# Optimization experiments

Hardware: AMD Instinct MI355X
Metric: run time of the kernel (lower is better)

The kernel has to match this reference:

```python
import jax, jax.numpy as jnp
import numpy as np

B, N, K = 8, 1024, 9
T = B * N
EPS_BN = 1e-5


def _knn_idx(x, k):
    # x: [n, d] -> [n, k] indices of k nearest neighbours (self included, dist 0)
    x = jax.lax.stop_gradient(x)
    sq = jnp.sum(x * x, axis=1)
    d = sq[:, None] + sq[None, :] - 2.0 * (x @ x.T)
    return jax.lax.top_k(-d, k)[1]


def _mlp_bn(x, params):
    # PyG MLP with plain_last=True: linear->BN->ReLU for all but last layer, last is linear.
    n = len(params)
    for i, (W, b, g, be) in enumerate(params):
        x = x @ W + b
        if i < n - 1:
            mu = jnp.mean(x, axis=0)
            var = jnp.var(x, axis=0)  # biased, as torch BN (training stats)
            x = g * (x - mu) * jax.lax.rsqrt(var + EPS_BN) + be
            x = jax.nn.relu(x)
    return x


def _edge_conv(x, idx, params):
    # DynamicEdgeConv: message = MLP([x_i, x_j - x_i]), aggr='mean' over k neighbours
    n, k = idx.shape
    xj = x[idx]                                   # [n,k,c] gather
    xi = jnp.broadcast_to(x[:, None, :], xj.shape)
    e = jnp.concatenate([xi, xj - xi], axis=-1).reshape(n * k, -1)
    h = _mlp_bn(e, params)                        # [n*k, c_out]
    return h.reshape(n, k, -1).mean(axis=1)       # mean aggregation


def _dgcnn(x, c1, c3, head, lin2_W, lin2_b):
    # conv1: kNN within each graph (batch-aware)
    xb = x.reshape(B, N, -1)
    idx = jax.vmap(lambda g: _knn_idx(g, K))(xb)                 # [B,N,K] local
    idx = (idx + (jnp.arange(B) * N)[:, None, None]).reshape(T, K)
    x1 = _edge_conv(x, idx, c1)                                  # [T,128]
    # head MLP (norm=None, dropout inactive in eval)
    h = x1
    for i, (W, b) in enumerate(head):
        h = h @ W + b
        if i < len(head) - 1:
            h = jax.nn.relu(h)
    out = (h - jnp.mean(h)) / (jnp.std(h, ddof=1) + 1e-5)        # torch.std unbiased
    out = jax.nn.sigmoid(out)                                    # [T,1] gate
    xl = out * x
    xs = (1.0 - out) * x
    # conv3 called without batch -> global kNN over all T nodes
    xl = _edge_conv(xl, _knn_idx(xl, K), c3)                     # [T,16]
    xs = _edge_conv(xs, _knn_idx(xs, K), c3)
    xl = xl.reshape(B, N, -1).max(axis=1)                        # global_max_pool
    xs = xs.reshape(B, N, -1).max(axis=1)
    mass = jnp.concatenate([xl, xs], axis=1) @ lin2_W + lin2_b   # [B,1]
    return mass.flatten()


_PARAM_SHAPES = {
    'c1_W1': (8, 128), 'c1_b1': (128,), 'c1_g1': (128,), 'c1_be1': (128,),
    'c1_W2': (128, 128), 'c1_b2': (128,), 'c1_g2': (128,), 'c1_be2': (128,),
    'c1_W3': (128, 128), 'c1_b3': (128,),
    'c3_W1': (8, 64), 'c3_b1': (64,), 'c3_g1': (64,), 'c3_be1': (64,),
    'c3_W2': (64, 64), 'c3_b2': (64,), 'c3_g2': (64,), 'c3_be2': (64,),
    'c3_W3': (64, 16), 'c3_b3': (16,),
    'h_W1': (128, 64), 'h_b1': (64,),
    'h_W2': (64, 32), 'h_b2': (32,),
    'h_W3': (32, 1), 'h_b3': (1,),
    'lin2_W': (32, 1), 'lin2_b': (1,),
}


def setup_inputs() -> dict:
    key = jax.random.key(0)
    ks = jax.random.split(key, len(_PARAM_SHAPES) + 1)
    inp = {'x': jax.random.normal(ks[0], (T, 4), dtype=jnp.float32)}
    for i, (name, shp) in enumerate(_PARAM_SHAPES.items()):
        v = jax.random.normal(ks[i + 1], shp, dtype=jnp.float32) * 0.1
        if '_g' in name:
            v = v + 1.0
        inp[name] = v
    return inp


def reference(x, c1_W1, c1_b1, c1_g1, c1_be1, c1_W2, c1_b2, c1_g2, c1_be2,
              c1_W3, c1_b3, c3_W1, c3_b1, c3_g1, c3_be1, c3_W2, c3_b2, c3_g2,
              c3_be2, c3_W3, c3_b3, h_W1, h_b1, h_W2, h_b2, h_W3, h_b3,
              lin2_W, lin2_b):
    c1 = [(c1_W1, c1_b1, c1_g1, c1_be1), (c1_W2, c1_b2, c1_g2, c1_be2),
          (c1_W3, c1_b3, None, None)]
    c3 = [(c3_W1, c3_b1, c3_g1, c3_be1), (c3_W2, c3_b2, c3_g2, c3_be2),
          (c3_W3, c3_b3, None, None)]
    head = [(h_W1, h_b1), (h_W2, h_b2), (h_W3, h_b3)]
    return _dgcnn(x, c1, c3, head, lin2_W, lin2_b)
```

## Files before the change

kernel.cpp:

```cpp
#include <hip/hip_runtime.h>
#include <math.h>

#define TN 8192
#define KNN 9
#define NPG 1024
#define TK (TN*KNN)
#define CPCL 12
#define NCHG 32
#define CPCG 16
#define NSYB 768

__device__ __forceinline__ float sqnorm(float4 v){
  return fmaf(v.x,v.x,fmaf(v.y,v.y,fmaf(v.z,v.z,v.w*v.w)));
}
__device__ __forceinline__ float pairdist(float4 a, float sqa, float4 b, float sqb){
  float dot = fmaf(a.x,b.x,fmaf(a.y,b.y,fmaf(a.z,b.z,a.w*b.w)));
  return sqa + sqb - 2.0f*dot;
}
__device__ __forceinline__ void chain9(float (&bd)[9], float d){
  float t=d;
  #pragma unroll
  for(int p=0;p<9;p++){
    float lo=fminf(bd[p],t);
    t=fmaxf(bd[p],t);
    bd[p]=lo;
  }
}
__device__ __forceinline__ void insert9(float (&bd)[9], int (&bi)[9], float d, int id){
  if(d < bd[8]){
    float td=d; int ti=id;
    #pragma unroll
    for(int p=0;p<9;p++){
      bool sw = (td < bd[p]);
      float nbd = sw ? td : bd[p];
      int   nbi = sw ? ti : bi[p];
      float ntd = sw ? bd[p] : td;
      int   nti = sw ? bi[p] : ti;
      bd[p]=nbd; bi[p]=nbi; td=ntd; ti=nti;
    }
  }
}

__global__ __launch_bounds__(256) void k_part_local(const float4* __restrict__ x, float* __restrict__ pd){
  __shared__ float4 sx[128]; __shared__ float ssq[128];
  int nb = blockIdx.x >> 3, chunk = blockIdx.x & 7;
  int g = nb >> 2;
  int cbase = g*NPG + chunk*128;
  if(threadIdx.x < 128){
    float4 v = x[cbase + threadIdx.x];
    sx[threadIdx.x]=v; ssq[threadIdx.x]=sqnorm(v);
  }
  __syncthreads();
  int node = nb*256 + threadIdx.x;
  float4 xi = x[node]; float sqi = sqnorm(xi);
  float bdA[9], bdB[9];
  #pragma unroll
  for(int q=0;q<9;q++){bdA[q]=1e30f;bdB[q]=1e30f;}
  for(int j=0;j<128;j+=2){
    chain9(bdA, pairdist(xi,sqi,sx[j],ssq[j]));
    chain9(bdB, pairdist(xi,sqi,sx[j+1],ssq[j+1]));
  }
  #pragma unroll
  for(int q=0;q<9;q++) chain9(bdA, bdB[q]);
  #pragma unroll
  for(int q=0;q<9;q++) pd[(size_t)(chunk*9+q)*TN + node]=bdA[q];
}

__global__ __launch_bounds__(256) void k_thresh_local(const float* __restrict__ pd,
      float* __restrict__ tl){
  int node = blockIdx.x*256 + threadIdx.x;
  float bd[9];
  #pragma unroll
  for(int q=0;q<9;q++) bd[q]=1e30f;
  for(int m=0;m<72;m++) chain9(bd, pd[(size_t)m*TN + node]);
  float t = bd[8];
  tl[node] = t + fabsf(t)*1e-5f + 1e-12f;
}

__global__ __launch_bounds__(256) void k_collect_local(const float4* __restrict__ x,
      const float* __restrict__ tl, unsigned char* __restrict__ cnt8,
      unsigned short* __restrict__ list){
  __shared__ float4 sx[128]; __shared__ float ssq[128];
  int nb = blockIdx.x >> 3, chunk = blockIdx.x & 7;
  int g = nb >> 2;
  int cbase = g*NPG + chunk*128;
  if(threadIdx.x < 128){
    float4 v = x[cbase + threadIdx.x];
    sx[threadIdx.x]=v; ssq[threadIdx.x]=sqnorm(v);
  }
  __syncthreads();
  int node = nb*256 + threadIdx.x;
  float4 xi = x[node];
  float m2x=-2.0f*xi.x, m2y=-2.0f*xi.y, m2z=-2.0f*xi.z, m2w=-2.0f*xi.w;
  float tadj = tl[node] - sqnorm(xi);
  int cnt = 0;
  unsigned short* lst = list + ((size_t)node*8 + chunk)*CPCL;
  for(int j=0;j<128;j+=4){
    float4 v0=sx[j], v1=sx[j+1], v2=sx[j+2], v3=sx[j+3];
    float q0=ssq[j], q1=ssq[j+1], q2=ssq[j+2], q3=ssq[j+3];
    float s0=fmaf(v0.x,m2x,fmaf(v0.y,m2y,fmaf(v0.z,m2z,fmaf(v0.w,m2w,q0))));
    float s1=fmaf(v1.x,m2x,fmaf(v1.y,m2y,fmaf(v1.z,m2z,fmaf(v1.w,m2w,q1))));
    float s2=fmaf(v2.x,m2x,fmaf(v2.y,m2y,fmaf(v2.z,m2z,fmaf(v2.w,m2w,q2))));
    float s3=fmaf(v3.x,m2x,fmaf(v3.y,m2y,fmaf(v3.z,m2z,fmaf(v3.w,m2w,q3))));
    if(s0<=tadj){ if(cnt<CPCL) lst[cnt]=(unsigned short)(cbase+j  ); cnt++; }
    if(s1<=tadj){ if(cnt<CPCL) lst[cnt]=(unsigned short)(cbase+j+1); cnt++; }
    if(s2<=tadj){ if(cnt<CPCL) lst[cnt]=(unsigned short)(cbase+j+2); cnt++; }
    if(s3<=tadj){ if(cnt<CPCL) lst[cnt]=(unsigned short)(cbase+j+3); cnt++; }
  }
  cnt8[(size_t)node*8 + chunk] = (unsigned char)(cnt > 255 ? 255 : cnt);
}

__global__ __launch_bounds__(256) void k_refine_local(const float4* __restrict__ x,
      const unsigned char* __restrict__ cnt8, const unsigned short* __restrict__ list,
      int* __restrict__ out){
  __shared__ float sval[32][73];
  __shared__ int   sidx[32][73];
  __shared__ int   sovf[32];
  int slot = threadIdx.x >> 3, sub = threadIdx.x & 7;
  int node = blockIdx.x*32 + slot;
  if(sub==0) sovf[slot]=0;
  __syncthreads();
  float4 xi = x[node]; float sqi = sqnorm(xi);
  float bd[9]; int bi[9];
  #pragma unroll
  for(int q=0;q<9;q++){bd[q]=1e30f; bi[q]=node;}
  int ch = sub;
  int c = cnt8[(size_t)node*8 + ch];
  if(c > CPCL) sovf[slot]=1;
  int n = c < CPCL ? c : CPCL;
  const unsigned short* lst = list + ((size_t)node*8 + ch)*CPCL;
  for(int m=0;m<n;m++){
    int j = lst[m]; float4 v = x[j];
    insert9(bd,bi, pairdist(xi,sqi,v,sqnorm(v)), j);
  }
  #pragma unroll
  for(int q=0;q<9;q++){ sval[slot][sub*9+q]=bd[q]; sidx[slot][sub*9+q]=bi[q]; }
  __syncthreads();
  if(sub==0){
    for(int m=9;m<72;m++) insert9(bd,bi, sval[slot][m], sidx[slot][m]);
    if(sovf[slot]){
      #pragma unroll
      for(int q=0;q<9;q++){bd[q]=1e30f; bi[q]=node;}
      int gbase = node & ~(NPG-1);
      for(int j=gbase;j<gbase+NPG;j++){
        float4 v = x[j];
        insert9(bd,bi, pairdist(xi,sqi,v,sqnorm(v)), j);
      }
    }
    #pragma unroll
    for(int q=0;q<9;q++) out[(size_t)node*9+q]=bi[q];
  }
}

__global__ __launch_bounds__(256) void k_part_sub(const float4* __restrict__ xa,
      const float4* __restrict__ xb, float* __restrict__ pd){
  const float4* x = blockIdx.y ? xb : xa;
  __shared__ float4 sx[256]; __shared__ float ssq[256];
  int nb = blockIdx.x >> 3, chunk = blockIdx.x & 7;
  {
    int j = (chunk*256 + threadIdx.x)*4;
    float4 v = x[j];
    sx[threadIdx.x]=v; ssq[threadIdx.x]=sqnorm(v);
  }
  __syncthreads();
  int node = nb*256 + threadIdx.x;
  float4 xi = x[node]; float sqi = sqnorm(xi);
  float bdA[9], bdB[9];
  #pragma unroll
  for(int q=0;q<9;q++){bdA[q]=1e30f;bdB[q]=1e30f;}
  for(int j=0;j<256;j+=2){
    chain9(bdA, pairdist(xi,sqi,sx[j],ssq[j]));
    chain9(bdB, pairdist(xi,sqi,sx[j+1],ssq[j+1]));
  }
  #pragma unroll
  for(int q=0;q<9;q++) chain9(bdA, bdB[q]);
  int pn = blockIdx.y*TN + node;
  #pragma unroll
  for(int q=0;q<9;q++) pd[(size_t)(chunk*9+q)*2*TN + pn]=bdA[q];
}

__global__ __launch_bounds__(256) void k_thresh_sub(const float* __restrict__ pd,
      float* __restrict__ tg){
  int pn = blockIdx.x*256 + threadIdx.x;
  float bd[9];
  #pragma unroll
  for(int q=0;q<9;q++) bd[q]=1e30f;
  for(int m=0;m<72;m++) chain9(bd, pd[(size_t)m*2*TN + pn]);
  float t = bd[8];
  tg[pn] = t + fabsf(t)*1e-5f + 1e-12f;
}

__global__ __launch_bounds__(256) void k_collect_glob(const float4* __restrict__ xa,
      const float4* __restrict__ xb, const float* __restrict__ tg,
      unsigned char* __restrict__ cnt8, unsigned short* __restrict__ list){
  const float4* x = blockIdx.y ? xb : xa;
  __shared__ float4 sx[256];
  __shared__ float4 ssq4[64];
  int nb = blockIdx.x >> 5, chunk = blockIdx.x & 31;
  int cbase = chunk*256;
  {
    float4 v = x[cbase+threadIdx.x];
    sx[threadIdx.x]=v; ((float*)ssq4)[threadIdx.x]=sqnorm(v);
  }
  __syncthreads();
  int node0 = nb*512 + threadIdx.x;
  int node1 = node0 + 256;
  int pn0 = blockIdx.y*TN + node0;
  int pn1 = pn0 + 256;
  float4 xi0 = x[node0], xi1 = x[node1];
  float a0x=-2.0f*xi0.x, a0y=-2.0f*xi0.y, a0z=-2.0f*xi0.z, a0w=-2.0f*xi0.w;
  float a1x=-2.0f*xi1.x, a1y=-2.0f*xi1.y, a1z=-2.0f*xi1.z, a1w=-2.0f*xi1.w;
  float t0 = tg[pn0] - sqnorm(xi0);
  float t1 = tg[pn1] - sqnorm(xi1);
  int c0 = 0, c1 = 0;
  unsigned short* l0 = list + ((size_t)pn0*NCHG + chunk)*CPCG;
  unsigned short* l1 = list + ((size_t)pn1*NCHG + chunk)*CPCG;
  for(int j=0;j<256;j+=4){
    float4 v0=sx[j], v1=sx[j+1], v2=sx[j+2], v3=sx[j+3];
    float4 qv = ssq4[j>>2];
    float s00=fmaf(v0.x,a0x,fmaf(v0.y,a0y,fmaf(v0.z,a0z,fmaf(v0.w,a0w,qv.x))));
    float s01=fmaf(v1.x,a0x,fmaf(v1.y,a0y,fmaf(v1.z,a0z,fmaf(v1.w,a0w,qv.y))));
    float s02=fmaf(v2.x,a0x,fmaf(v2.y,a0y,fmaf(v2.z,a0z,fmaf(v2.w,a0w,qv.z))));
    float s03=fmaf(v3.x,a0x,fmaf(v3.y,a0y,fmaf(v3.z,a0z,fmaf(v3.w,a0w,qv.w))));
    float s10=fmaf(v0.x,a1x,fmaf(v0.y,a1y,fmaf(v0.z,a1z,fmaf(v0.w,a1w,qv.x))));
    float s11=fmaf(v1.x,a1x,fmaf(v1.y,a1y,fmaf(v1.z,a1z,fmaf(v1.w,a1w,qv.y))));
    float s12=fmaf(v2.x,a1x,fmaf(v2.y,a1y,fmaf(v2.z,a1z,fmaf(v2.w,a1w,qv.z))));
    float s13=fmaf(v3.x,a1x,fmaf(v3.y,a1y,fmaf(v3.z,a1z,fmaf(v3.w,a1w,qv.w))));
    if(s00<=t0){ if(c0<CPCG) l0[c0]=(unsigned short)(cbase+j  ); c0++; }
    if(s01<=t0){ if(c0<CPCG) l0[c0]=(unsigned short)(cbase+j+1); c0++; }
    if(s02<=t0){ if(c0<CPCG) l0[c0]=(unsigned short)(cbase+j+2); c0++; }
    if(s03<=t0){ if(c0<CPCG) l0[c0]=(unsigned short)(cbase+j+3); c0++; }
    if(s10<=t1){ if(c1<CPCG) l1[c1]=(unsigned short)(cbase+j  ); c1++; }
    if(s11<=t1){ if(c1<CPCG) l1[c1]=(unsigned short)(cbase+j+1); c1++; }
    if(s12<=t1){ if(c1<CPCG) l1[c1]=(unsigned short)(cbase+j+2); c1++; }
    if(s13<=t1){ if(c1<CPCG) l1[c1]=(unsigned short)(cbase+j+3); c1++; }
  }
  cnt8[(size_t)pn0*NCHG + chunk] = (unsigned char)(c0 > 255 ? 255 : c0);
  cnt8[(size_t)pn1*NCHG + chunk] = (unsigned char)(c1 > 255 ? 255 : c1);
}

__global__ __launch_bounds__(256) void k_refine_glob(const float4* __restrict__ xa,
      const float4* __restrict__ xb, const unsigned char* __restrict__ cnt8,
      const unsigned short* __restrict__ list, int* __restrict__ outl, int* __restrict__ outs){
  __shared__ float sval[32][73];
  __shared__ int   sidx[32][73];
  __shared__ int   sovf[32];
  int slot = threadIdx.x >> 3, sub = threadIdx.x & 7;
  int pn = blockIdx.x*32 + slot;
  int prob = blockIdx.x >> 8;
  int node = pn & (TN-1);
  const float4* x = prob ? xb : xa;
  if(sub==0) sovf[slot]=0;
  __syncthreads();
  float4 xi = x[node]; float sqi = sqnorm(xi);
  float bd[9]; int bi[9];
  #pragma unroll
  for(int q=0;q<9;q++){bd[q]=1e30f; bi[q]=node;}
  bool ovf=false;
  for(int ch=sub*4; ch<sub*4+4; ch++){
    int c = cnt8[(size_t)pn*NCHG + ch];
    if(c > CPCG) ovf=true;
    int n = c < CPCG ? c : CPCG;
    const unsigned short* lst = list + ((size_t)pn*NCHG + ch)*CPCG;
    for(int m=0;m<n;m++){
      int j = lst[m]; float4 v = x[j];
      insert9(bd,bi, pairdist(xi,sqi,v,sqnorm(v)), j);
    }
  }
  if(ovf) sovf[slot]=1;
  #pragma unroll
  for(int q=0;q<9;q++){ sval[slot][sub*9+q]=bd[q]; sidx[slot][sub*9+q]=bi[q]; }
  __syncthreads();
  if(sub==0){
    for(int m=9;m<72;m++) insert9(bd,bi, sval[slot][m], sidx[slot][m]);
    if(sovf[slot]){
      #pragma unroll
      for(int q=0;q<9;q++){bd[q]=1e30f; bi[q]=node;}
      for(int j=0;j<TN;j++){
        float4 v = x[j];
        insert9(bd,bi, pairdist(xi,sqi,v,sqnorm(v)), j);
      }
    }
    int* o = prob ? outs : outl;
    #pragma unroll
    for(int q=0;q<9;q++) o[(size_t)node*9+q]=bi[q];
  }
}

__global__ __launch_bounds__(256) void k_mom8(const float4* __restrict__ x,
      const int* __restrict__ idx, float* __restrict__ mpart){
  __shared__ float sa[256][9];
  int t = threadIdx.x;
  int e = blockIdx.x*256 + t;
  int i = e/KNN; int j = idx[e];
  float4 xi = x[i], xj = x[j];
  sa[t][0]=xi.x; sa[t][1]=xi.y; sa[t][2]=xi.z; sa[t][3]=xi.w;
  sa[t][4]=xj.x-xi.x; sa[t][5]=xj.y-xi.y; sa[t][6]=xj.z-xi.z; sa[t][7]=xj.w-xi.w;
  __syncthreads();
  if(t < 44){
    float s=0.f;
    if(t<8){
      for(int e2=0;e2<256;e2++) s += sa[e2][t];
    } else {
      int f=t-8, p=0, q=0, acc=0;
      for(p=0;p<8;p++){ int cnt=8-p; if(f<acc+cnt){ q=p+(f-acc); break;} acc+=cnt; }
      for(int e2=0;e2<256;e2++) s += sa[e2][p]*sa[e2][q];
    }
    mpart[blockIdx.x*44+t]=s;
  }
}

__global__ void k_bn1q(const float* __restrict__ mpart, const float* __restrict__ W1,
      const float* __restrict__ g, const float* __restrict__ be,
      float* __restrict__ scale, float* __restrict__ shift){
  __shared__ double mom[44];
  int t = threadIdx.x;
  if(t<44){ double s=0; for(int b=0;b<288;b++) s+=(double)mpart[b*44+t]; mom[t]=s; }
  __syncthreads();
  double m[8], w[8];
  #pragma unroll
  for(int p=0;p<8;p++){ m[p]=mom[p]/(double)TK; w[p]=(double)W1[p*128+t]; }
  double q=0.0; int f=8;
  for(int p=0;p<8;p++)
    for(int qq=p;qq<8;qq++){
      double cov = mom[f]/(double)TK - m[p]*m[qq];
      q += (p==qq?1.0:2.0)*w[p]*w[qq]*cov;
      f++;
    }
  if(q<0) q=0;
  double sc = (double)g[t]/sqrt(q+1e-5);
  double mu=0; for(int p=0;p<8;p++) mu += m[p]*w[p];
  scale[t]=(float)sc;
  shift[t]=(float)((double)be[t] - mu*sc);
}

__global__ __launch_bounds__(256) void k_syrk128(const float4* __restrict__ x,
      const int* __restrict__ idx, const float* __restrict__ W1,
      const float* __restrict__ sc1, const float* __restrict__ sh1,
      float* __restrict__ mpartM){
  __shared__ float sa[48][9];
  __shared__ float sW1[8*128];
  __shared__ float sZ[48*132];
  __shared__ float ssum[128];
  const int tid = threadIdx.x;
  ((float4*)sW1)[tid] = ((const float4*)W1)[tid];
  if(tid<128) ssum[tid]=0.f;
  const int zc4 = tid & 31, ze0 = tid >> 5;
  const int gi = tid >> 4, gj = tid & 15;
  const int ia = gi*4, ib = 64 + gi*4;
  const int ja = gj*4, jb = 64 + gj*4;
  float acc[8][8];
  #pragma unroll
  for(int a=0;a<8;a++)
    #pragma unroll
    for(int b=0;b<8;b++) acc[a][b]=0.f;
  float ls[4]={0,0,0,0};
  float4 scv = ((const float4*)sc1)[zc4];
  float4 shv = ((const float4*)sh1)[zc4];
  for(int pass=0;pass<2;pass++){
    __syncthreads();
    if(tid<48){
      int e = blockIdx.x*96 + pass*48 + tid;
      int i = e/KNN; int j = idx[e];
      float4 xi = x[i], xj = x[j];
      sa[tid][0]=xi.x; sa[tid][1]=xi.y; sa[tid][2]=xi.z; sa[tid][3]=xi.w;
      sa[tid][4]=xj.x-xi.x; sa[tid][5]=xj.y-xi.y; sa[tid][6]=xj.z-xi.z; sa[tid][7]=xj.w-xi.w;
    }
    __syncthreads();
    for(int e=ze0; e<48; e+=8){
      float4 y = make_float4(0.f,0.f,0.f,0.f);
      #pragma unroll
      for(int k=0;k<8;k++){
        float a = sa[e][k];
        float4 wv = *(const float4*)(sW1 + k*128 + zc4*4);
        y.x=fmaf(a,wv.x,y.x); y.y=fmaf(a,wv.y,y.y);
        y.z=fmaf(a,wv.z,y.z); y.w=fmaf(a,wv.w,y.w);
      }
      float4 z;
      z.x = fmaxf(fmaf(scv.x,y.x,shv.x),0.f);
      z.y = fmaxf(fmaf(scv.y,y.y,shv.y),0.f);
      z.z = fmaxf(fmaf(scv.z,y.z,shv.z),0.f);
      z.w = fmaxf(fmaf(scv.w,y.w,shv.w),0.f);
      *(float4*)(sZ + e*132 + zc4*4) = z;
      ls[0]+=z.x; ls[1]+=z.y; ls[2]+=z.z; ls[3]+=z.w;
    }
    __syncthreads();
    #pragma unroll 2
    for(int e=0;e<48;e++){
      const float* rz = sZ + e*132;
      float4 zi0 = *(const float4*)(rz + ia);
      float4 zi1 = *(const float4*)(rz + ib);
      float4 zj0 = *(const float4*)(rz + ja);
      float4 zj1 = *(const float4*)(rz + jb);
      float zi[8] = {zi0.x,zi0.y,zi0.z,zi0.w,zi1.x,zi1.y,zi1.z,zi1.w};
      float zj[8] = {zj0.x,zj0.y,zj0.z,zj0.w,zj1.x,zj1.y,zj1.z,zj1.w};
      #pragma unroll
      for(int a=0;a<8;a++)
        #pragma unroll
        for(int b=0;b<8;b++) acc[a][b]=fmaf(zi[a],zj[b],acc[a][b]);
    }
  }
  #pragma unroll
  for(int c=0;c<4;c++) atomicAdd(&ssum[zc4*4+c], ls[c]);
  float* mp = mpartM + (size_t)blockIdx.x*16512;
  #pragma unroll
  for(int a=0;a<8;a++){
    int row = (a<4) ? (ia+a) : (ib+a-4);
    *(float4*)(mp + row*128 + ja) = make_float4(acc[a][0],acc[a][1],acc[a][2],acc[a][3]);
    *(float4*)(mp + row*128 + jb) = make_float4(acc[a][4],acc[a][5],acc[a][6],acc[a][7]);
  }
  __syncthreads();
  if(tid<128) mp[16384+tid] = ssum[tid];
}

__global__ __launch_bounds__(256) void k_redA(const float* __restrict__ mpartM,
      double* __restrict__ pp8){
  int ch = blockIdx.x*256 + threadIdx.x;
  if(ch >= 16512) return;
  int y = blockIdx.y;
  double s=0;
  for(int b=y*96;b<y*96+96;b++) s += (double)mpartM[(size_t)b*16512 + ch];
  pp8[(size_t)y*16512 + ch]=s;
}

__global__ __launch_bounds__(256) void k_redB(const double* __restrict__ pp8,
      double* __restrict__ Md){
  int ch = blockIdx.x*256 + threadIdx.x;
  if(ch >= 16512) return;
  double s=0;
  #pragma unroll
  for(int y=0;y<8;y++) s += pp8[(size_t)y*16512 + ch];
  Md[ch]=s;
}

__global__ void k_bn2q(const double* __restrict__ Md, const float* __restrict__ W2,
      const float* __restrict__ g, const float* __restrict__ be,
      float* __restrict__ scale, float* __restrict__ shift){
  __shared__ double redq[128], redt[128];
  __shared__ float sw[128];
  int c = blockIdx.x, t = threadIdx.x;
  sw[t] = W2[t*128+c];
  __syncthreads();
  double zb = Md[16384+t]/(double)TK;
  double inner=0;
  for(int j=0;j<128;j++) inner += Md[t*128+j]*(double)sw[j];
  redq[t] = (double)sw[t]*(inner/(double)TK);
  redt[t] = (double)sw[t]*zb;
  __syncthreads();
  for(int s=64;s>0;s>>=1){
    if(t<s){ redq[t]+=redq[t+s]; redt[t]+=redt[t+s]; }
    __syncthreads();
  }
  if(t==0){
    double var = redq[0] - redt[0]*redt[0];
    if(var<0) var=0;
    double sc = (double)g[c]/sqrt(var+1e-5);
    scale[c]=(float)sc;
    shift[c]=(float)((double)be[c] - redt[0]*sc);
  }
}

__global__ __launch_bounds__(256) void k_midagg(const float4* __restrict__ x,
      const int* __restrict__ idx, const float* __restrict__ W1,
      const float* __restrict__ sc1, const float* __restrict__ sh1,
      const float* __restrict__ W2, const float* __restrict__ sc2,
      const float* __restrict__ sh2, const float* __restrict__ W3,
      const float* __restrict__ b3, float* __restrict__ x1){
  __shared__ float sa[72][9];
  __shared__ float sW1[8*128];
  __shared__ float sZ[72*68];
  const int tid = threadIdx.x;
  const int node0 = blockIdx.x*8;
  ((float4*)sW1)[tid] = ((const float4*)W1)[tid];
  if(tid<72){
    int e = blockIdx.x*72 + tid;
    int i = e/KNN; int j = idx[e];
    float4 xi = x[i], xj = x[j];
    sa[tid][0]=xi.x; sa[tid][1]=xi.y; sa[tid][2]=xi.z; sa[tid][3]=xi.w;
    sa[tid][4]=xj.x-xi.x; sa[tid][5]=xj.y-xi.y; sa[tid][6]=xj.z-xi.z; sa[tid][7]=xj.w-xi.w;
  }
  __syncthreads();
  const int tc = tid & 31, tr = tid >> 5;
  float acc[9][4];
  #pragma unroll
  for(int s=0;s<9;s++)
    #pragma unroll
    for(int e=0;e<4;e++) acc[s][e]=0.f;
  for(int half=0; half<2; half++){
    for(int f=tid; f<72*16; f+=256){
      int e = f>>4, c4 = f&15;
      int gc4 = half*16 + c4;
      float4 scv = ((const float4*)sc1)[gc4];
      float4 shv = ((const float4*)sh1)[gc4];
      float4 y = make_float4(0.f,0.f,0.f,0.f);
      #pragma unroll
      for(int k=0;k<8;k++){
        float a = sa[e][k];
        float4 wv = *(const float4*)(sW1 + k*128 + gc4*4);
        y.x=fmaf(a,wv.x,y.x); y.y=fmaf(a,wv.y,y.y);
        y.z=fmaf(a,wv.z,y.z); y.w=fmaf(a,wv.w,y.w);
      }
      float4 z;
      z.x = fmaxf(fmaf(scv.x,y.x,shv.x),0.f);
      z.y = fmaxf(fmaf(scv.y,y.y,shv.y),0.f);
      z.z = fmaxf(fmaf(scv.z,y.z,shv.z),0.f);
      z.w = fmaxf(fmaf(scv.w,y.w,shv.w),0.f);
      *(float4*)(sZ + e*68 + c4*4) = z;
    }
    __syncthreads();
    #pragma unroll 2
    for(int k4=0;k4<16;k4++){
      float4 av[9];
      #pragma unroll
      for(int s=0;s<9;s++) av[s] = *(const float4*)(sZ + (tr*9+s)*68 + k4*4);
      #pragma unroll
      for(int kk=0;kk<4;kk++){
        float4 bv = *(const float4*)(W2 + (size_t)(half*64 + k4*4+kk)*128 + tc*4);
        #pragma unroll
        for(int s=0;s<9;s++){
          float a = (kk==0)?av[s].x:(kk==1)?av[s].y:(kk==2)?av[s].z:av[s].w;
          acc[s][0]=fmaf(a,bv.x,acc[s][0]);
          acc[s][1]=fmaf(a,bv.y,acc[s][1]);
          acc[s][2]=fmaf(a,bv.z,acc[s][2]);
          acc[s][3]=fmaf(a,bv.w,acc[s][3]);
        }
      }
    }
    __syncthreads();
  }
  float4 scv = ((const float4*)sc2)[tc];
  float4 shv = ((const float4*)sh2)[tc];
  float4 sum = make_float4(0.f,0.f,0.f,0.f);
  #pragma unroll
  for(int s=0;s<9;s++){
    sum.x += fmaxf(fmaf(scv.x,acc[s][0],shv.x),0.f);
    sum.y += fmaxf(fmaf(scv.y,acc[s][1],shv.y),0.f);
    sum.z += fmaxf(fmaf(scv.z,acc[s][2],shv.z),0.f);
    sum.w += fmaxf(fmaf(scv.w,acc[s][3],shv.w),0.f);
  }
  sum.x*=(1.f/9.f); sum.y*=(1.f/9.f); sum.z*=(1.f/9.f); sum.w*=(1.f/9.f);
  *(float4*)(sZ + tr*132 + tc*4) = sum;
  __syncthreads();
  const float* zr = sZ + tr*132;
  float4 o = make_float4(0.f,0.f,0.f,0.f);
  #pragma unroll 4
  for(int k=0;k<128;k++){
    float a = zr[k];
    float4 bv = *(const float4*)(W3 + (size_t)k*128 + tc*4);
    o.x=fmaf(a,bv.x,o.x); o.y=fmaf(a,bv.y,o.y);
    o.z=fmaf(a,bv.z,o.z); o.w=fmaf(a,bv.w,o.w);
  }
  float4 bb = ((const float4*)b3)[tc];
  o.x+=bb.x; o.y+=bb.y; o.z+=bb.z; o.w+=bb.w;
  *(float4*)(x1 + (size_t)(node0+tr)*128 + tc*4) = o;
}

__global__ __launch_bounds__(256) void k_mom8d(const float4* __restrict__ xa,
      const float4* __restrict__ xb, const int* __restrict__ ia,
      const int* __restrict__ ib, float* __restrict__ mpart){
  __shared__ float sa[256][9];
  const int prob = blockIdx.y;
  const float4* x = prob ? xb : xa;
  const int* idx = prob ? ib : ia;
  int t = threadIdx.x;
  int e = blockIdx.x*256 + t;
  int i = e/KNN; int j = idx[e];
  float4 xi = x[i], xj = x[j];
  sa[t][0]=xi.x; sa[t][1]=xi.y; sa[t][2]=xi.z; sa[t][3]=xi.w;
  sa[t][4]=xj.x-xi.x; sa[t][5]=xj.y-xi.y; sa[t][6]=xj.z-xi.z; sa[t][7]=xj.w-xi.w;
  __syncthreads();
  if(t < 44){
    float s=0.f;
    if(t<8){
      for(int e2=0;e2<256;e2++) s += sa[e2][t];
    } else {
      int f=t-8, p=0, q=0, acc=0;
      for(p=0;p<8;p++){ int cnt=8-p; if(f<acc+cnt){ q=p+(f-acc); break;} acc+=cnt; }
      for(int e2=0;e2<256;e2++) s += sa[e2][p]*sa[e2][q];
    }
    mpart[((size_t)prob*288 + blockIdx.x)*44 + t]=s;
  }
}

__global__ void k_bn1qd(const float* __restrict__ mpart, const float* __restrict__ W1,
      const float* __restrict__ g, const float* __restrict__ be,
      float* __restrict__ scale, float* __restrict__ shift){
  __shared__ double mom[2][44];
  int t = threadIdx.x;
  if(t<88){
    int pr=t/44, m=t%44;
    double s=0; for(int b=0;b<288;b++) s+=(double)mpart[((size_t)pr*288+b)*44+m];
    mom[pr][m]=s;
  }
  __syncthreads();
  int prob = t>>6, c = t&63;
  double m[8], w[8];
  #pragma unroll
  for(int p=0;p<8;p++){ m[p]=mom[prob][p]/(double)TK; w[p]=(double)W1[p*64+c]; }
  double q=0.0; int f=8;
  for(int p=0;p<8;p++)
    for(int qq=p;qq<8;qq++){
      double cov = mom[prob][f]/(double)TK - m[p]*m[qq];
      q += (p==qq?1.0:2.0)*w[p]*w[qq]*cov;
      f++;
    }
  if(q<0) q=0;
  double sc = (double)g[c]/sqrt(q+1e-5);
  double mu=0; for(int p=0;p<8;p++) mu += m[p]*w[p];
  scale[prob*64+c]=(float)sc;
  shift[prob*64+c]=(float)((double)be[c] - mu*sc);
}

__global__ __launch_bounds__(256) void k_syrk64d(const float4* __restrict__ xa,
      const float4* __restrict__ xb, const int* __restrict__ ia,
      const int* __restrict__ ib, const float* __restrict__ W1,
      const float* __restrict__ sc0, const float* __restrict__ sh0,
      float* __restrict__ mpartM){
  __shared__ float sa[64][9];
  __shared__ float sW1[8*64];
  __shared__ float sZ[64*68];
  __shared__ float ssum[64];
  const int prob = blockIdx.y;
  const float4* x = prob ? xb : xa;
  const int* idx = prob ? ib : ia;
  const float* sc1 = sc0 + prob*64;
  const float* sh1 = sh0 + prob*64;
  const int tid = threadIdx.x;
  if(tid<128) ((float4*)sW1)[tid] = ((const float4*)W1)[tid];
  if(tid<64) ssum[tid]=0.f;
  const int zc4 = tid & 15, ze0 = tid >> 4;
  const int i0 = (tid>>4)*4, j0 = (tid&15)*4;
  float acc[4][4];
  #pragma unroll
  for(int a=0;a<4;a++)
    #pragma unroll
    for(int b=0;b<4;b++) acc[a][b]=0.f;
  float ls[4]={0,0,0,0};
  float4 scv = ((const float4*)sc1)[zc4];
  float4 shv = ((const float4*)sh1)[zc4];
  for(int pass=0;pass<4;pass++){
    __syncthreads();
    if(tid<64){
      int e = blockIdx.x*256 + pass*64 + tid;
      int i = e/KNN; int j = idx[e];
      float4 xi = x[i], xj = x[j];
      sa[tid][0]=xi.x; sa[tid][1]=xi.y; sa[tid][2]=xi.z; sa[tid][3]=xi.w;
      sa[tid][4]=xj.x-xi.x; sa[tid][5]=xj.y-xi.y; sa[tid][6]=xj.z-xi.z; sa[tid][7]=xj.w-xi.w;
    }
    __syncthreads();
    for(int e=ze0; e<64; e+=16){
      float4 y = make_float4(0.f,0.f,0.f,0.f);
      #pragma unroll
      for(int k=0;k<8;k++){
        float a = sa[e][k];
        float4 wv = *(const float4*)(sW1 + k*64 + zc4*4);
        y.x=fmaf(a,wv.x,y.x); y.y=fmaf(a,wv.y,y.y);
        y.z=fmaf(a,wv.z,y.z); y.w=fmaf(a,wv.w,y.w);
      }
      float4 z;
      z.x = fmaxf(fmaf(scv.x,y.x,shv.x),0.f);
      z.y = fmaxf(fmaf(scv.y,y.y,shv.y),0.f);
      z.z = fmaxf(fmaf(scv.z,y.z,shv.z),0.f);
      z.w = fmaxf(fmaf(scv.w,y.w,shv.w),0.f);
      *(float4*)(sZ + e*68 + zc4*4) = z;
      ls[0]+=z.x; ls[1]+=z.y; ls[2]+=z.z; ls[3]+=z.w;
    }
    __syncthreads();
    #pragma unroll 4
    for(int e=0;e<64;e++){
      const float* rz = sZ + e*68;
      float4 zi4 = *(const float4*)(rz + i0);
      float4 zj4 = *(const float4*)(rz + j0);
      float zi[4]={zi4.x,zi4.y,zi4.z,zi4.w};
      float zj[4]={zj4.x,zj4.y,zj4.z,zj4.w};
      #pragma unroll
      for(int a=0;a<4;a++)
        #pragma unroll
        for(int b=0;b<4;b++) acc[a][b]=fmaf(zi[a],zj[b],acc[a][b]);
    }
  }
  #pragma unroll
  for(int c=0;c<4;c++) atomicAdd(&ssum[zc4*4+c], ls[c]);
  float* mp = mpartM + ((size_t)prob*288 + blockIdx.x)*4160;
  #pragma unroll
  for(int a=0;a<4;a++)
    *(float4*)(mp + (i0+a)*64 + j0) = make_float4(acc[a][0],acc[a][1],acc[a][2],acc[a][3]);
  __syncthreads();
  if(tid<64) mp[4096+tid] = ssum[tid];
}

__global__ __launch_bounds__(256) void k_redMd(const float* __restrict__ mpartM,
      double* __restrict__ Md){
  int ch = blockIdx.x*256 + threadIdx.x;
  if(ch >= 8320) return;
  int prob = ch / 4160, c = ch % 4160;
  double s=0;
  for(int b=0;b<288;b++) s += (double)mpartM[((size_t)prob*288+b)*4160 + c];
  Md[(size_t)prob*4160 + c]=s;
}

__global__ void k_bn2qd(const double* __restrict__ Md, const float* __restrict__ W2,
      const float* __restrict__ g, const float* __restrict__ be,
      float* __restrict__ scale, float* __restrict__ shift){
  __shared__ double redq[64], redt[64];
  __shared__ float sw[64];
  int c = blockIdx.x, prob = blockIdx.y, t = threadIdx.x;
  const double* md = Md + (size_t)prob*4160;
  sw[t] = W2[t*64+c];
  __syncthreads();
  double zb = md[4096+t]/(double)TK;
  double inner=0;
  for(int j=0;j<64;j++) inner += md[t*64+j]*(double)sw[j];
  redq[t] = (double)sw[t]*(inner/(double)TK);
  redt[t] = (double)sw[t]*zb;
  __syncthreads();
  for(int s=32;s>0;s>>=1){
    if(t<s){ redq[t]+=redq[t+s]; redt[t]+=redt[t+s]; }
    __syncthreads();
  }
  if(t==0){
    double var = redq[0] - redt[0]*redt[0];
    if(var<0) var=0;
    double sc = (double)g[c]/sqrt(var+1e-5);
    scale[prob*64+c]=(float)sc;
    shift[prob*64+c]=(float)((double)be[c] - redt[0]*sc);
  }
}

__global__ __launch_bounds__(256) void k_midagg64d(const float4* __restrict__ xa,
      const float4* __restrict__ xb, const int* __restrict__ ia,
      const int* __restrict__ ib, const float* __restrict__ W1,
      const float* __restrict__ sc0, const float* __restrict__ sh0,
      const float* __restrict__ W2, const float* __restrict__ sc20,
      const float* __restrict__ sh20, const float* __restrict__ W3,
      const float* __restrict__ b3, float* __restrict__ outl, float* __restrict__ outs){
  __shared__ float sa[144][9];
  __shared__ float sW1[8*64];
  __shared__ float sZ[144*36];
  const int prob = blockIdx.y;
  const float4* x = prob ? xb : xa;
  const int* idx = prob ? ib : ia;
  const float* sc1 = sc0 + prob*64;
  const float* sh1 = sh0 + prob*64;
  const float* sc2 = sc20 + prob*64;
  const float* sh2 = sh20 + prob*64;
  float* out = prob ? outs : outl;
  const int tid = threadIdx.x;
  const int node0 = blockIdx.x*16;
  if(tid<128) ((float4*)sW1)[tid] = ((const float4*)W1)[tid];
  if(tid<144){
    int e = blockIdx.x*144 + tid;
    int i = e/KNN; int j = idx[e];
    float4 xi = x[i], xj = x[j];
    sa[tid][0]=xi.x; sa[tid][1]=xi.y; sa[tid][2]=xi.z; sa[tid][3]=xi.w;
    sa[tid][4]=xj.x-xi.x; sa[tid][5]=xj.y-xi.y; sa[tid][6]=xj.z-xi.z; sa[tid][7]=xj.w-xi.w;
  }
  __syncthreads();
  const int cg = tid & 15, nd = tid >> 4;
  float acc[9][4];
  #pragma unroll
  for(int s=0;s<9;s++)
    #pragma unroll
    for(int e=0;e<4;e++) acc[s][e]=0.f;
  for(int half=0; half<2; half++){
    for(int f=tid; f<144*8; f+=256){
      int e = f>>3, c4 = f&7;
      int gc4 = half*8 + c4;
      float4 scv = ((const float4*)sc1)[gc4];
      float4 shv = ((const float4*)sh1)[gc4];
      float4 y = make_float4(0.f,0.f,0.f,0.f);
      #pragma unroll
      for(int k=0;k<8;k++){
        float a = sa[e][k];
        float4 wv = *(const float4*)(sW1 + k*64 + gc4*4);
        y.x=fmaf(a,wv.x,y.x); y.y=fmaf(a,wv.y,y.y);
        y.z=fmaf(a,wv.z,y.z); y.w=fmaf(a,wv.w,y.w);
      }
      float4 z;
      z.x = fmaxf(fmaf(scv.x,y.x,shv.x),0.f);
      z.y = fmaxf(fmaf(scv.y,y.y,shv.y),0.f);
      z.z = fmaxf(fmaf(scv.z,y.z,shv.z),0.f);
      z.w = fmaxf(fmaf(scv.w,y.w,shv.w),0.f);
      *(float4*)(sZ + e*36 + c4*4) = z;
    }
    __syncthreads();
    #pragma unroll 2
    for(int k4=0;k4<8;k4++){
      float4 av[9];
      #pragma unroll
      for(int s=0;s<9;s++) av[s] = *(const float4*)(sZ + (nd*9+s)*36 + k4*4);
      #pragma unroll
      for(int kk=0;kk<4;kk++){
        float4 bv = *(const float4*)(W2 + (size_t)(half*32 + k4*4+kk)*64 + cg*4);
        #pragma unroll
        for(int s=0;s<9;s++){
          float a = (kk==0)?av[s].x:(kk==1)?av[s].y:(kk==2)?av[s].z:av[s].w;
          acc[s][0]=fmaf(a,bv.x,acc[s][0]);
          acc[s][1]=fmaf(a,bv.y,acc[s][1]);
          acc[s][2]=fmaf(a,bv.z,acc[s][2]);
          acc[s][3]=fmaf(a,bv.w,acc[s][3]);
        }
      }
    }
    __syncthreads();
  }
  float4 scv = ((const float4*)sc2)[cg];
  float4 shv = ((const float4*)sh2)[cg];
  float4 sum = make_float4(0.f,0.f,0.f,0.f);
  #pragma unroll
  for(int s=0;s<9;s++){
    sum.x += fmaxf(fmaf(scv.x,acc[s][0],shv.x),0.f);
    sum.y += fmaxf(fmaf(scv.y,acc[s][1],shv.y),0.f);
    sum.z += fmaxf(fmaf(scv.z,acc[s][2],shv.z),0.f);
    sum.w += fmaxf(fmaf(scv.w,acc[s][3],shv.w),0.f);
  }
  sum.x*=(1.f/9.f); sum.y*=(1.f/9.f); sum.z*=(1.f/9.f); sum.w*=(1.f/9.f);
  *(float4*)(sZ + nd*68 + cg*4) = sum;
  __syncthreads();
  {
    int node = tid >> 4, col = tid & 15;
    const float* zr = sZ + node*68;
    float o = 0.f;
    #pragma unroll 4
    for(int k=0;k<64;k++) o = fmaf(zr[k], W3[k*16+col], o);
    out[(size_t)(node0+node)*16 + col] = o + b3[col];
  }
}

__global__ __launch_bounds__(256) void k_head(const float* __restrict__ x1,
    const float* __restrict__ W1, const float* __restrict__ b1,
    const float* __restrict__ W2, const float* __restrict__ b2,
    const float* __restrict__ W3, const float* __restrict__ b3,
    float* __restrict__ h, float* __restrict__ pstat){
  __shared__ float sA[32*132];
  __shared__ float sW1[128*64];
  __shared__ float o1[32*68];
  __shared__ float sW2[64*32];
  __shared__ float o2[32*33];
  __shared__ float sb1[64], sb2[32], sW3v[32];
  __shared__ float rs[32], rq[32];
  const int tid = threadIdx.x;
  const int row0 = blockIdx.x*32;
  for(int e=tid; e<32*32; e+=256){
    int r = e>>5, c4 = e&31;
    ((float4*)(sA + r*132))[c4] = ((const float4*)(x1 + (size_t)(row0+r)*128))[c4];
  }
  for(int e=tid; e<128*64/4; e+=256) ((float4*)sW1)[e] = ((const float4*)W1)[e];
  for(int e=tid; e<64*32/4; e+=256)  ((float4*)sW2)[e] = ((const float4*)W2)[e];
  if(tid < 64) sb1[tid]=b1[tid];
  if(tid < 32){ sb2[tid]=b2[tid]; sW3v[tid]=W3[tid]; }
  __syncthreads();
  const int tc = tid & 15, tr = tid >> 4;
  float a1[2][4];
  #pragma unroll
  for(int rr=0;rr<2;rr++)
    #pragma unroll
    for(int e=0;e<4;e++) a1[rr][e]=0.f;
  for(int k4=0;k4<32;k4++){
    float4 av0 = *(const float4*)(sA + (tr*2  )*132 + k4*4);
    float4 av1 = *(const float4*)(sA + (tr*2+1)*132 + k4*4);
    #pragma unroll
    for(int kk=0;kk<4;kk++){
      float4 bv = *(const float4*)(sW1 + (k4*4+kk)*64 + tc*4);
      float p0 = (kk==0)?av0.x:(kk==1)?av0.y:(kk==2)?av0.z:av0.w;
      float p1 = (kk==0)?av1.x:(kk==1)?av1.y:(kk==2)?av1.z:av1.w;
      a1[0][0]=fmaf(p0,bv.x,a1[0][0]); a1[0][1]=fmaf(p0,bv.y,a1[0][1]);
      a1[0][2]=fmaf(p0,bv.z,a1[0][2]); a1[0][3]=fmaf(p0,bv.w,a1[0][3]);
      a1[1][0]=fmaf(p1,bv.x,a1[1][0]); a1[1][1]=fmaf(p1,bv.y,a1[1][1]);
      a1[1][2]=fmaf(p1,bv.z,a1[1][2]); a1[1][3]=fmaf(p1,bv.w,a1[1][3]);
    }
  }
  #pragma unroll
  for(int rr=0;rr<2;rr++)
    #pragma unroll
    for(int e=0;e<4;e++)
      o1[(tr*2+rr)*68 + tc*4+e] = fmaxf(a1[rr][e]+sb1[tc*4+e], 0.f);
  __syncthreads();
  float a2[2][2] = {{0.f,0.f},{0.f,0.f}};
  for(int k=0;k<64;k++){
    float w0 = sW2[k*32 + tc*2], w1 = sW2[k*32 + tc*2+1];
    float v0 = o1[(tr*2  )*68 + k];
    float v1 = o1[(tr*2+1)*68 + k];
    a2[0][0]=fmaf(v0,w0,a2[0][0]); a2[0][1]=fmaf(v0,w1,a2[0][1]);
    a2[1][0]=fmaf(v1,w0,a2[1][0]); a2[1][1]=fmaf(v1,w1,a2[1][1]);
  }
  #pragma unroll
  for(int rr=0;rr<2;rr++)
    #pragma unroll
    for(int cc=0;cc<2;cc++)
      o2[(tr*2+rr)*33 + tc*2+cc] = fmaxf(a2[rr][cc]+sb2[tc*2+cc], 0.f);
  __syncthreads();
  if(tid < 32){
    float hv = b3[0];
    #pragma unroll
    for(int k=0;k<32;k++) hv = fmaf(o2[tid*33+k], sW3v[k], hv);
    h[row0+tid]=hv;
    rs[tid]=hv; rq[tid]=hv*hv;
  }
  __syncthreads();
  if(tid==0){
    float S=0.f, Q=0.f;
    #pragma unroll
    for(int i=0;i<32;i++){ S+=rs[i]; Q+=rq[i]; }
    pstat[blockIdx.x*2]=S; pstat[blockIdx.x*2+1]=Q;
  }
}

__global__ __launch_bounds__(256) void k_fin_h(const float* __restrict__ pstat,
      float* __restrict__ hpar){
  __shared__ double sS[256], sQ[256];
  int t = threadIdx.x;
  sS[t] = (double)pstat[2*t]; sQ[t] = (double)pstat[2*t+1];
  __syncthreads();
  for(int s=128;s>0;s>>=1){
    if(t<s){ sS[t]+=sS[t+s]; sQ[t]+=sQ[t+s]; }
    __syncthreads();
  }
  if(t==0){
    double mu = sS[0]/8192.0;
    double var = (sQ[0] - 8192.0*mu*mu)/8191.0;
    double sd = (var > 0) ? sqrt(var) : 0.0;
    hpar[0]=(float)mu;
    hpar[1]=(float)(1.0/(sd + 1e-5));
  }
}

__global__ __launch_bounds__(256) void k_gate(const float* __restrict__ h,
      const float* __restrict__ hpar, const float4* __restrict__ x,
      float4* __restrict__ xl, float4* __restrict__ xs){
  int i = blockIdx.x*256 + threadIdx.x;
  float z = (h[i]-hpar[0])*hpar[1];
  float o = 1.0f/(1.0f+expf(-z));
  float om = 1.0f - o;
  float4 v = x[i];
  xl[i] = make_float4(o*v.x, o*v.y, o*v.z, o*v.w);
  xs[i] = make_float4(om*v.x, om*v.y, om*v.z, om*v.w);
}

__global__ __launch_bounds__(256) void k_final(const float* __restrict__ xlf,
      const float* __restrict__ xsf, const float* __restrict__ W,
      const float* __restrict__ b, float* __restrict__ out){
  __shared__ float red[32][8];
  int g = blockIdx.x;
  int c = threadIdx.x & 31;
  int chunk = threadIdx.x >> 5;
  const float* src = (c < 16) ? xlf : xsf;
  int ch = (c < 16) ? c : c-16;
  float m = -1e30f;
  for(int n=chunk*128; n<chunk*128+128; n++)
    m = fmaxf(m, src[((size_t)g*1024+n)*16 + ch]);
  red[c][chunk]=m;
  __syncthreads();
  if(threadIdx.x < 32){
    float mm = red[threadIdx.x][0];
    #pragma unroll
    for(int p=1;p<8;p++) mm = fmaxf(mm, red[threadIdx.x][p]);
    red[threadIdx.x][0]=mm;
  }
  __syncthreads();
  if(threadIdx.x == 0){
    float acc = b[0];
    for(int cc=0;cc<32;cc++) acc = fmaf(red[cc][0], W[cc], acc);
    out[g]=acc;
  }
}

extern "C" void kernel_launch(void* const* d_in, const int* in_sizes, int n_in,
                              void* d_out, int out_size, void* d_ws, size_t ws_size,
                              hipStream_t stream){
  const float* x    =(const float*)d_in[0];
  const float* c1W1 =(const float*)d_in[1];
  const float* c1g1 =(const float*)d_in[3];
  const float* c1be1=(const float*)d_in[4];
  const float* c1W2 =(const float*)d_in[5];
  const float* c1g2 =(const float*)d_in[7];
  const float* c1be2=(const float*)d_in[8];
  const float* c1W3 =(const float*)d_in[9];
  const float* c1b3 =(const float*)d_in[10];
  const float* c3W1 =(const float*)d_in[11];
  const float* c3g1 =(const float*)d_in[13];
  const float* c3be1=(const float*)d_in[14];
  const float* c3W2 =(const float*)d_in[15];
  const float* c3g2 =(const float*)d_in[17];
  const float* c3be2=(const float*)d_in[18];
  const float* c3W3 =(const float*)d_in[19];
  const float* c3b3 =(const float*)d_in[20];
  const float* hW1  =(const float*)d_in[21];
  const float* hb1  =(const float*)d_in[22];
  const float* hW2  =(const float*)d_in[23];
  const float* hb2  =(const float*)d_in[24];
  const float* hW3  =(const float*)d_in[25];
  const float* hb3  =(const float*)d_in[26];
  const float* l2W  =(const float*)d_in[27];
  const float* l2b  =(const float*)d_in[28];
  (void)in_sizes; (void)n_in; (void)out_size; (void)ws_size;

  char* wsb=(char*)d_ws;
  size_t off=0;
  auto alloc=[&](size_t bytes)->char*{
    char* p = wsb + off;
    off = (off + bytes + 255) & ~(size_t)255;
    return p;
  };
  float* ovl  =(float*)alloc((size_t)NSYB*16512*4);
  float* x1   =(float*)alloc((size_t)TN*128*4);
  int*   idx1 =(int*)  alloc((size_t)TK*4);
  int*   idxl =(int*)  alloc((size_t)TK*4);
  int*   idxs =(int*)  alloc((size_t)TK*4);
  float* pd   =(float*)alloc((size_t)2*TN*72*4);
  float* h    =(float*)alloc((size_t)TN*4);
  float* xl   =(float*)alloc((size_t)TN*16);
  float* xs   =(float*)alloc((size_t)TN*16);
  float* xlf  =(float*)alloc((size_t)TN*16*4);
  float* xsf  =(float*)alloc((size_t)TN*16*4);
  float* pstat=(float*)alloc((size_t)512*4);
  double* Md  =(double*)alloc((size_t)16512*8);
  double* Mdd =(double*)alloc((size_t)8320*8);
  double* pp8 =(double*)alloc((size_t)8*16512*8);
  float* mp44 =(float*)alloc((size_t)288*44*4);
  float* mp44d=(float*)alloc((size_t)2*288*44*4);
  float* tl   =(float*)alloc((size_t)TN*4);
  float* tg   =(float*)alloc((size_t)2*TN*4);
  unsigned char* cnt8l=(unsigned char*)alloc((size_t)TN*8);
  unsigned char* cnt8g=(unsigned char*)alloc((size_t)2*TN*NCHG);
  float* bnp  =(float*)alloc(1024*4);
  float* hpar =(float*)alloc(64);

  float* sc1=bnp,      *sh1=bnp+128, *sc2=bnp+256, *sh2=bnp+384;
  float* scA=bnp+512,  *shA=bnp+640, *scB=bnp+768, *shB=bnp+896;
  unsigned short* listl=(unsigned short*)ovl;
  unsigned short* listg=(unsigned short*)ovl;
  float* mpartM = ovl;
  float* mpartMd = ovl;

  k_part_local  <<<256,256,0,stream>>>((const float4*)x, pd);
  k_thresh_local<<<32, 256,0,stream>>>(pd, tl);
  k_collect_local<<<256,256,0,stream>>>((const float4*)x, tl, cnt8l, listl);
  k_refine_local<<<TN/32,256,0,stream>>>((const float4*)x, cnt8l, listl, idx1);
  k_mom8<<<288,256,0,stream>>>((const float4*)x, idx1, mp44);
  k_bn1q<<<1,128,0,stream>>>(mp44, c1W1, c1g1, c1be1, sc1, sh1);
  k_syrk128<<<NSYB,256,0,stream>>>((const float4*)x, idx1, c1W1, sc1, sh1, mpartM);
  k_redA<<<dim3(65,8),256,0,stream>>>(mpartM, pp8);
  k_redB<<<65,256,0,stream>>>(pp8, Md);
  k_bn2q<<<128,128,0,stream>>>(Md, c1W2, c1g2, c1be2, sc2, sh2);
  k_midagg<<<1024,256,0,stream>>>((const float4*)x, idx1, c1W1, sc1, sh1, c1W2, sc2, sh2, c1W3, c1b3, x1);
  k_head<<<TN/32,256,0,stream>>>(x1,hW1,hb1,hW2,hb2,hW3,hb3,h,pstat);
  k_fin_h<<<1,256,0,stream>>>(pstat,hpar);
  k_gate<<<32,256,0,stream>>>(h,hpar,(const float4*)x,(float4*)xl,(float4*)xs);
  k_part_sub   <<<dim3(256,2),256,0,stream>>>((const float4*)xl,(const float4*)xs,pd);
  k_thresh_sub <<<64,256,0,stream>>>(pd,tg);
  k_collect_glob<<<dim3(512,2),256,0,stream>>>((const float4*)xl,(const float4*)xs,tg,cnt8g,listg);
  k_refine_glob<<<2*TN/32,256,0,stream>>>((const float4*)xl,(const float4*)xs,cnt8g,listg,idxl,idxs);
  k_mom8d<<<dim3(288,2),256,0,stream>>>((const float4*)xl,(const float4*)xs,idxl,idxs,mp44d);
  k_bn1qd<<<1,128,0,stream>>>(mp44d, c3W1, c3g1, c3be1, scA, shA);
  k_syrk64d<<<dim3(288,2),256,0,stream>>>((const float4*)xl,(const float4*)xs,idxl,idxs,c3W1,scA,shA,mpartMd);
  k_redMd<<<33,256,0,stream>>>(mpartMd, Mdd);
  k_bn2qd<<<dim3(64,2),64,0,stream>>>(Mdd, c3W2, c3g2, c3be2, scB, shB);
  k_midagg64d<<<dim3(512,2),256,0,stream>>>((const float4*)xl,(const float4*)xs,idxl,idxs,
      c3W1, scA, shA, c3W2, scB, shB, c3W3, c3b3, xlf, xsf);
  k_final<<<8,256,0,stream>>>(xlf,xsf,l2W,l2b,(float*)d_out);
}
```

Before: 407.8 us.

## Retile k_midagg to 16 nodes per block with 8 output columns per thread

k_midagg now handles 16 nodes (144 edges) per block instead of 8, and each thread computes 8 output channels for one node instead of 4. The hidden layer is processed in four 32-channel quarters rather than two 64-channel halves, which shrinks the shared staging buffer. The aim is to halve the W2/W3 global reads per edge and raise FMA work per load. In exchange each thread holds twice the accumulators (72 floats), which raises register pressure, and the grid shrinks to 512 blocks.

Result: no change. 409.8 us (+0.5%).

```diff
diff --git a/kernel.cpp b/kernel.cpp
--- a/kernel.cpp
+++ b/kernel.cpp
@@ -466,30 +466,30 @@
       const float* __restrict__ W2, const float* __restrict__ sc2,
       const float* __restrict__ sh2, const float* __restrict__ W3,
       const float* __restrict__ b3, float* __restrict__ x1){
-  __shared__ float sa[72][9];
+  __shared__ float sa[144][9];
   __shared__ float sW1[8*128];
-  __shared__ float sZ[72*68];
+  __shared__ float sZ[144*36];
   const int tid = threadIdx.x;
-  const int node0 = blockIdx.x*8;
+  const int node0 = blockIdx.x*16;
   ((float4*)sW1)[tid] = ((const float4*)W1)[tid];
-  if(tid<72){
-    int e = blockIdx.x*72 + tid;
+  if(tid<144){
+    int e = blockIdx.x*144 + tid;
     int i = e/KNN; int j = idx[e];
     float4 xi = x[i], xj = x[j];
     sa[tid][0]=xi.x; sa[tid][1]=xi.y; sa[tid][2]=xi.z; sa[tid][3]=xi.w;
     sa[tid][4]=xj.x-xi.x; sa[tid][5]=xj.y-xi.y; sa[tid][6]=xj.z-xi.z; sa[tid][7]=xj.w-xi.w;
   }
   __syncthreads();
-  const int tc = tid & 31, tr = tid >> 5;
-  float acc[9][4];
+  const int cg = tid & 15, nd = tid >> 4;
+  float acc[9][8];
   #pragma unroll
   for(int s=0;s<9;s++)
     #pragma unroll
-    for(int e=0;e<4;e++) acc[s][e]=0.f;
-  for(int half=0; half<2; half++){
-    for(int f=tid; f<72*16; f+=256){
-      int e = f>>4, c4 = f&15;
-      int gc4 = half*16 + c4;
+    for(int e=0;e<8;e++) acc[s][e]=0.f;
+  for(int q=0;q<4;q++){
+    for(int f=tid; f<144*8; f+=256){
+      int e = f>>3, c4 = f&7;
+      int gc4 = q*8 + c4;
       float4 scv = ((const float4*)sc1)[gc4];
       float4 shv = ((const float4*)sh1)[gc4];
       float4 y = make_float4(0.f,0.f,0.f,0.f);
@@ -505,54 +505,76 @@
       z.y = fmaxf(fmaf(scv.y,y.y,shv.y),0.f);
       z.z = fmaxf(fmaf(scv.z,y.z,shv.z),0.f);
       z.w = fmaxf(fmaf(scv.w,y.w,shv.w),0.f);
-      *(float4*)(sZ + e*68 + c4*4) = z;
+      *(float4*)(sZ + e*36 + c4*4) = z;
     }
     __syncthreads();
     #pragma unroll 2
-    for(int k4=0;k4<16;k4++){
-      float4 av[9];
-      #pragma unroll
-      for(int s=0;s<9;s++) av[s] = *(const float4*)(sZ + (tr*9+s)*68 + k4*4);
+    for(int k4=0;k4<8;k4++){
+      float4 bv0[4], bv1[4];
       #pragma unroll
       for(int kk=0;kk<4;kk++){
-        float4 bv = *(const float4*)(W2 + (size_t)(half*64 + k4*4+kk)*128 + tc*4);
+        const float* wr = W2 + (size_t)(q*32 + k4*4 + kk)*128 + cg*8;
+        bv0[kk] = *(const float4*)(wr);
+        bv1[kk] = *(const float4*)(wr + 4);
+      }
+      #pragma unroll
+      for(int s=0;s<9;s++){
+        float4 av = *(const float4*)(sZ + (nd*9+s)*36 + k4*4);
         #pragma unroll
-        for(int s=0;s<9;s++){
-          float a = (kk==0)?av[s].x:(kk==1)?av[s].y:(kk==2)?av[s].z:av[s].w;
-          acc[s][0]=fmaf(a,bv.x,acc[s][0]);
-          acc[s][1]=fmaf(a,bv.y,acc[s][1]);
-          acc[s][2]=fmaf(a,bv.z,acc[s][2]);
-          acc[s][3]=fmaf(a,bv.w,acc[s][3]);
+        for(int kk=0;kk<4;kk++){
+          float a = (kk==0)?av.x:(kk==1)?av.y:(kk==2)?av.z:av.w;
+          acc[s][0]=fmaf(a,bv0[kk].x,acc[s][0]);
+          acc[s][1]=fmaf(a,bv0[kk].y,acc[s][1]);
+          acc[s][2]=fmaf(a,bv0[kk].z,acc[s][2]);
+          acc[s][3]=fmaf(a,bv0[kk].w,acc[s][3]);
+          acc[s][4]=fmaf(a,bv1[kk].x,acc[s][4]);
+          acc[s][5]=fmaf(a,bv1[kk].y,acc[s][5]);
+          acc[s][6]=fmaf(a,bv1[kk].z,acc[s][6]);
+          acc[s][7]=fmaf(a,bv1[kk].w,acc[s][7]);
         }
       }
     }
     __syncthreads();
   }
-  float4 scv = ((const float4*)sc2)[tc];
-  float4 shv = ((const float4*)sh2)[tc];
-  float4 sum = make_float4(0.f,0.f,0.f,0.f);
+  float4 scv0 = ((const float4*)sc2)[cg*2],   shv0 = ((const float4*)sh2)[cg*2];
+  float4 scv1 = ((const float4*)sc2)[cg*2+1], shv1 = ((const float4*)sh2)[cg*2+1];
+  float4 sum0 = make_float4(0.f,0.f,0.f,0.f);
+  float4 sum1 = make_float4(0.f,0.f,0.f,0.f);
   #pragma unroll
   for(int s=0;s<9;s++){
-    sum.x += fmaxf(fmaf(scv.x,acc[s][0],shv.x),0.f);
-    sum.y += fmaxf(fmaf(scv.y,acc[s][1],shv.y),0.f);
-    sum.z += fmaxf(fmaf(scv.z,acc[s][2],shv.z),0.f);
-    sum.w += fmaxf(fmaf(scv.w,acc[s][3],shv.w),0.f);
-  }
-  sum.x*=(1.f/9.f); sum.y*=(1.f/9.f); sum.z*=(1.f/9.f); sum.w*=(1.f/9.f);
-  *(float4*)(sZ + tr*132 + tc*4) = sum;
-  __syncthreads();
-  const float* zr = sZ + tr*132;
-  float4 o = make_float4(0.f,0.f,0.f,0.f);
+    sum0.x += fmaxf(fmaf(scv0.x,acc[s][0],shv0.x),0.f);
+    sum0.y += fmaxf(fmaf(scv0.y,acc[s][1],shv0.y),0.f);
+    sum0.z += fmaxf(fmaf(scv0.z,acc[s][2],shv0.z),0.f);
+    sum0.w += fmaxf(fmaf(scv0.w,acc[s][3],shv0.w),0.f);
+    sum1.x += fmaxf(fmaf(scv1.x,acc[s][4],shv1.x),0.f);
+    sum1.y += fmaxf(fmaf(scv1.y,acc[s][5],shv1.y),0.f);
+    sum1.z += fmaxf(fmaf(scv1.z,acc[s][6],shv1.z),0.f);
+    sum1.w += fmaxf(fmaf(scv1.w,acc[s][7],shv1.w),0.f);
+  }
+  sum0.x*=(1.f/9.f); sum0.y*=(1.f/9.f); sum0.z*=(1.f/9.f); sum0.w*=(1.f/9.f);
+  sum1.x*=(1.f/9.f); sum1.y*=(1.f/9.f); sum1.z*=(1.f/9.f); sum1.w*=(1.f/9.f);
+  *(float4*)(sZ + nd*132 + cg*8)     = sum0;
+  *(float4*)(sZ + nd*132 + cg*8 + 4) = sum1;
+  __syncthreads();
+  const float* zr = sZ + nd*132;
+  float4 o0 = make_float4(0.f,0.f,0.f,0.f);
+  float4 o1 = make_float4(0.f,0.f,0.f,0.f);
   #pragma unroll 4
   for(int k=0;k<128;k++){
     float a = zr[k];
-    float4 bv = *(const float4*)(W3 + (size_t)k*128 + tc*4);
-    o.x=fmaf(a,bv.x,o.x); o.y=fmaf(a,bv.y,o.y);
-    o.z=fmaf(a,bv.z,o.z); o.w=fmaf(a,bv.w,o.w);
-  }
-  float4 bb = ((const float4*)b3)[tc];
-  o.x+=bb.x; o.y+=bb.y; o.z+=bb.z; o.w+=bb.w;
-  *(float4*)(x1 + (size_t)(node0+tr)*128 + tc*4) = o;
+    const float* wr = W3 + (size_t)k*128 + cg*8;
+    float4 bv0 = *(const float4*)(wr);
+    float4 bv1 = *(const float4*)(wr + 4);
+    o0.x=fmaf(a,bv0.x,o0.x); o0.y=fmaf(a,bv0.y,o0.y);
+    o0.z=fmaf(a,bv0.z,o0.z); o0.w=fmaf(a,bv0.w,o0.w);
+    o1.x=fmaf(a,bv1.x,o1.x); o1.y=fmaf(a,bv1.y,o1.y);
+    o1.z=fmaf(a,bv1.z,o1.z); o1.w=fmaf(a,bv1.w,o1.w);
+  }
+  float4 bb0 = ((const float4*)b3)[cg*2], bb1 = ((const float4*)b3)[cg*2+1];
+  o0.x+=bb0.x; o0.y+=bb0.y; o0.z+=bb0.z; o0.w+=bb0.w;
+  o1.x+=bb1.x; o1.y+=bb1.y; o1.z+=bb1.z; o1.w+=bb1.w;
+  *(float4*)(x1 + (size_t)(node0+nd)*128 + cg*8)     = o0;
+  *(float4*)(x1 + (size_t)(node0+nd)*128 + cg*8 + 4) = o1;
 }
 
 __global__ __launch_bounds__(256) void k_mom8d(const float4* __restrict__ xa,
@@ -1043,7 +1065,7 @@
   k_redA<<<dim3(65,8),256,0,stream>>>(mpartM, pp8);
   k_redB<<<65,256,0,stream>>>(pp8, Md);
   k_bn2q<<<128,128,0,stream>>>(Md, c1W2, c1g2, c1be2, sc2, sh2);
-  k_midagg<<<1024,256,0,stream>>>((const float4*)x, idx1, c1W1, sc1, sh1, c1W2, sc2, sh2, c1W3, c1b3, x1);
+  k_midagg<<<512,256,0,stream>>>((const float4*)x, idx1, c1W1, sc1, sh1, c1W2, sc2, sh2, c1W3, c1b3, x1);
   k_head<<<TN/32,256,0,stream>>>(x1,hW1,hb1,hW2,hb2,hW3,hb3,h,pstat);
   k_fin_h<<<1,256,0,stream>>>(pstat,hpar);
   k_gate<<<32,256,0,stream>>>(h,hpar,(const float4*)x,(float4*)xl,(float4*)xs);
```
